# Kernel optimization log

Hardware: AMD Instinct MI355X
Metric: run time of the kernel (lower is better)

## Reference

```python
import jax, jax.numpy as jnp
import numpy as np

D_MODEL = 5120
N_HEADS = 8
D_HEAD = D_MODEL // N_HEADS          # 640
D_ROPE = 16
SPLIT_DIM = D_HEAD - D_ROPE          # 624
D_KV = 128
BATCH, SEQ = 2, 2048
ROPE_SCALE = 40.0


def _rope_cos_sin(seq_len):
    # inv_freq length = D_ROPE//4 (quirk of the original code)
    inv_freq = 1.0 / (10000.0 ** (jnp.arange(0, D_ROPE // 2, 2, dtype=jnp.float32) / (D_ROPE // 2)))
    t = jnp.arange(seq_len, dtype=jnp.float32) / ROPE_SCALE
    freqs = t[:, None] * inv_freq[None, :]            # [S, D_ROPE//4]
    emb = jnp.concatenate([freqs, freqs], axis=-1)    # [S, D_ROPE//2]
    cos = jnp.cos(emb)[None, :, None, :]              # [1,S,1,D_ROPE//2]
    sin = jnp.sin(emb)[None, :, None, :]
    return cos, sin


def _rotate_half(x):
    x1, x2 = jnp.split(x, 2, axis=-1)
    return jnp.concatenate([-x2, x1], axis=-1)


def _apply_rotary(x, cos, sin):
    r = cos.shape[-1]
    x_rot, x_base = x[..., :r], x[..., r:]
    x_rot = x_rot * cos + _rotate_half(x_rot) * sin
    return jnp.concatenate([x_rot, x_base], axis=-1)


def setup_inputs():
    key = jax.random.key(0)
    ks = jax.random.split(key, 18)
    s = 0.02
    inp = {
        'h': jax.random.normal(ks[0], (BATCH, SEQ, D_MODEL), dtype=jnp.float32),
        'W_dkv': jax.random.normal(ks[1], (D_MODEL, D_KV), dtype=jnp.float32) * s,
        'b_dkv': jnp.zeros((D_KV,), jnp.float32),
        'W_dq': jax.random.normal(ks[2], (D_MODEL, D_KV), dtype=jnp.float32) * s,
        'b_dq': jnp.zeros((D_KV,), jnp.float32),
        'W_uk': jax.random.normal(ks[3], (D_KV, N_HEADS * SPLIT_DIM), dtype=jnp.float32) * s,
        'b_uk': jnp.zeros((N_HEADS * SPLIT_DIM,), jnp.float32),
        'W_uv': jax.random.normal(ks[4], (D_KV, N_HEADS * D_HEAD), dtype=jnp.float32) * s,
        'b_uv': jnp.zeros((N_HEADS * D_HEAD,), jnp.float32),
        'W_uq': jax.random.normal(ks[5], (D_KV, N_HEADS * SPLIT_DIM), dtype=jnp.float32) * s,
        'b_uq': jnp.zeros((N_HEADS * SPLIT_DIM,), jnp.float32),
        'W_qr': jax.random.normal(ks[6], (D_KV, N_HEADS * D_ROPE), dtype=jnp.float32) * s,
        'b_qr': jnp.zeros((N_HEADS * D_ROPE,), jnp.float32),
        'W_kr': jax.random.normal(ks[7], (D_MODEL, N_HEADS * D_ROPE), dtype=jnp.float32) * s,
        'b_kr': jnp.zeros((N_HEADS * D_ROPE,), jnp.float32),
        'W_o': jax.random.normal(ks[8], (N_HEADS * D_HEAD, D_MODEL), dtype=jnp.float32) * s,
        'b_o': jnp.zeros((D_MODEL,), jnp.float32),
    }
    return inp


def reference(h, W_dkv, b_dkv, W_dq, b_dq, W_uk, b_uk, W_uv, b_uv,
              W_uq, b_uq, W_qr, b_qr, W_kr, b_kr, W_o, b_o):
    B, S, _ = h.shape
    c_kv = h @ W_dkv + b_dkv                                   # [B,S,D_KV]
    k = (c_kv @ W_uk + b_uk).reshape(B, S, N_HEADS, SPLIT_DIM)
    v = (c_kv @ W_uv + b_uv).reshape(B, S, N_HEADS, D_HEAD)
    c_q = h @ W_dq + b_dq
    q_base = (c_q @ W_uq + b_uq).reshape(B, S, N_HEADS, SPLIT_DIM)
    q_rot = (c_q @ W_qr + b_qr).reshape(B, S, N_HEADS, D_ROPE)
    cos, sin = _rope_cos_sin(S)
    q_rot = _apply_rotary(q_rot, cos, sin)
    k_rot = _apply_rotary((h @ W_kr + b_kr).reshape(B, S, N_HEADS, D_ROPE), cos, sin)
    q = jnp.concatenate([q_base, q_rot], axis=-1)              # [B,S,H,D_HEAD]
    k = jnp.concatenate([k, k_rot], axis=-1)                   # [B,S,H,D_HEAD]
    scores = jnp.einsum('bqhd,bkhd->bhqk', q, k) / jnp.sqrt(jnp.float32(D_HEAD))
    attn = jax.nn.softmax(scores, axis=-1)
    out = jnp.einsum('bhqk,bkhd->bqhd', attn, v)               # [B,S,H,D_HEAD]
    return out.reshape(B, S, N_HEADS * D_HEAD) @ W_o + b_o
```

## Files before the change

kernel.cpp:

```cpp
#include <hip/hip_runtime.h>


typedef unsigned short ushort_t;
typedef __attribute__((ext_vector_type(8)))  short          short8;
typedef __attribute__((ext_vector_type(8)))  unsigned short us8;
typedef __attribute__((ext_vector_type(4)))  float          f32x4;
typedef __attribute__((ext_vector_type(4)))  unsigned int   u32x4;

#define SCALE_ATT 0.0395284707521047f

static __device__ inline unsigned short f2bf(float f) {
  union { float f; unsigned u; } v; v.f = f;
  unsigned r = (v.u + 0x7fffu + ((v.u >> 16) & 1u)) >> 16;
  return (unsigned short)r;
}
static __device__ inline float bf2f(unsigned short u) {
  union { unsigned u; float f; } v; v.u = ((unsigned)u) << 16;
  return v.f;
}
static __device__ inline unsigned cvt_pk_bf16(float a, float b) {
  unsigned r;
  asm("v_cvt_pk_bf16_f32 %0, %1, %2" : "=v"(r) : "v"(a), "v"(b));
  return r;
}
static __device__ inline f32x4 MFMA(short8 a, short8 b, f32x4 c) {
  return __builtin_amdgcn_mfma_f32_16x16x32_bf16(a, b, c, 0, 0, 0);
}

__global__ __launch_bounds__(256) void k_bvec_init(const float* __restrict__ bo,
                                                   float* __restrict__ bvec) {
  int n = blockIdx.x * 256 + threadIdx.x;
  bvec[n] = bo[n];
}

__global__ __launch_bounds__(128) void k_bqabs(const float* __restrict__ buq,
                                               const float* __restrict__ Wuk,
                                               float* __restrict__ bqabs) {
  int h = blockIdx.x, j = threadIdx.x;
  float acc = 0.f;
  const float* bq = buq + h * 624;
  const float* wk = Wuk + (size_t)j * 4992 + h * 624;
  for (int d = 0; d < 624; ++d) acc += bq[d] * wk[d];
  bqabs[h * 128 + j] = acc;
}

__global__ __launch_bounds__(256) void k_wqk(const float* __restrict__ Wuq,
                                             const float* __restrict__ Wuk,
                                             ushort_t* __restrict__ wqkT) {
  __shared__ float Aq[16 * 132];
  __shared__ float Ak[16 * 132];
  int jt = blockIdx.x, it = blockIdx.y, h = blockIdx.z;
  int i0 = it * 16, j0 = jt * 16;
  int t = threadIdx.x;
  int srow = t >> 4, sc0 = (t & 15) * 8;
  int ti = t & 15, tj = t >> 4;
  float acc = 0.f;
  for (int dc = 0; dc < 624; dc += 128) {
#pragma unroll
    for (int i = 0; i < 8; ++i) {
      int d = dc + sc0 + i;
      Aq[srow * 132 + sc0 + i] = (d < 624) ? Wuq[(size_t)(i0 + srow) * 4992 + h * 624 + d] : 0.f;
      Ak[srow * 132 + sc0 + i] = (d < 624) ? Wuk[(size_t)(j0 + srow) * 4992 + h * 624 + d] : 0.f;
    }
    __syncthreads();
    int cs = (624 - dc) < 128 ? (624 - dc) : 128;
    for (int d = 0; d < cs; d += 4) {
      const f32x4 a4 = *(const f32x4*)&Aq[ti * 132 + d];
      const f32x4 b4 = *(const f32x4*)&Ak[tj * 132 + d];
      acc += a4[0] * b4[0] + a4[1] * b4[1] + a4[2] * b4[2] + a4[3] * b4[3];
    }
    __syncthreads();
  }
  wqkT[(size_t)h * 16384 + (size_t)(j0 + tj) * 128 + (i0 + ti)] = f2bf(acc);
}

__global__ __launch_bounds__(256) void k_gemm1_sk(
    const float* __restrict__ H, const float* __restrict__ Wdkv,
    const float* __restrict__ Wdq, const float* __restrict__ Wkr,
    float* __restrict__ part) {
  __shared__ __align__(16) ushort_t As[64 * 72];
  __shared__ __align__(16) ushort_t Bs[192 * 72];
  const int tid = threadIdx.x;
  const int m0 = blockIdx.x * 64;
  const int n0 = blockIdx.y * 192;
  const int kc0 = blockIdx.z * 1280;
  const int lane = tid & 63, wid = tid >> 6;
  const int quad = lane >> 4, l15 = lane & 15;
  f32x4 acc[4][3];
#pragma unroll
  for (int a = 0; a < 4; ++a)
#pragma unroll
    for (int b = 0; b < 3; ++b) acc[a][b] = (f32x4){0.f, 0.f, 0.f, 0.f};
  const int ar = tid >> 2, ak0 = (tid & 3) * 16;
  const int bkp = tid >> 3;
  const int bng = tid & 7;
  const float* harow = H + (size_t)(m0 + ar) * 5120 + ak0;
  for (int kb = kc0; kb < kc0 + 1280; kb += 64) {
    const float* ap = harow + kb;
    f32x4 af0 = *(const f32x4*)ap, af1 = *(const f32x4*)(ap + 4);
    f32x4 af2 = *(const f32x4*)(ap + 8), af3 = *(const f32x4*)(ap + 12);
    u32x4 apk0 = { cvt_pk_bf16(af0[0], af0[1]), cvt_pk_bf16(af0[2], af0[3]),
                   cvt_pk_bf16(af1[0], af1[1]), cvt_pk_bf16(af1[2], af1[3]) };
    u32x4 apk1 = { cvt_pk_bf16(af2[0], af2[1]), cvt_pk_bf16(af2[2], af2[3]),
                   cvt_pk_bf16(af3[0], af3[1]), cvt_pk_bf16(af3[2], af3[3]) };
    *(u32x4*)&As[ar * 72 + ak0] = apk0;
    *(u32x4*)&As[ar * 72 + ak0 + 8] = apk1;
    const int krow = kb + 2 * bkp;
    const int kd = (2 * bkp) ^ (bng << 3);
#pragma unroll
    for (int g = 0; g < 3; ++g) {
      const int lcol = g * 64 + bng * 8;
      const int col = n0 + lcol;
      const float* base = (col < 128 ? Wdkv + col
                         : col < 256 ? Wdq + (col - 128)
                                     : Wkr + (col - 256)) + (size_t)krow * 128;
      f32x4 r0a = *(const f32x4*)base, r0b = *(const f32x4*)(base + 4);
      f32x4 r1a = *(const f32x4*)(base + 128), r1b = *(const f32x4*)(base + 132);
#pragma unroll
      for (int i = 0; i < 4; ++i) {
        *(unsigned*)&Bs[(lcol + i) * 72 + kd]     = cvt_pk_bf16(r0a[i], r1a[i]);
        *(unsigned*)&Bs[(lcol + 4 + i) * 72 + kd] = cvt_pk_bf16(r0b[i], r1b[i]);
      }
    }
    __syncthreads();
#pragma unroll
    for (int ks = 0; ks < 2; ++ks) {
      short8 a[4], b[3];
#pragma unroll
      for (int mt = 0; mt < 4; ++mt)
        a[mt] = *(const short8*)&As[(mt * 16 + l15) * 72 + ks * 32 + quad * 8];
#pragma unroll
      for (int nt = 0; nt < 3; ++nt) {
        const int row = wid * 48 + nt * 16 + l15;
        const int kofs = (ks * 32 + quad * 8) ^ (((row >> 3) & 7) << 3);
        b[nt] = *(const short8*)&Bs[row * 72 + kofs];
      }
#pragma unroll
      for (int mt = 0; mt < 4; ++mt)
#pragma unroll
        for (int nt = 0; nt < 3; ++nt) acc[mt][nt] = MFMA(a[mt], b[nt], acc[mt][nt]);
    }
    __syncthreads();
  }
  const size_t pb = (size_t)blockIdx.z * 4096 * 384;
#pragma unroll
  for (int mt = 0; mt < 4; ++mt)
#pragma unroll
    for (int nt = 0; nt < 3; ++nt) {
      const int col = n0 + wid * 48 + nt * 16 + l15;
#pragma unroll
      for (int r = 0; r < 4; ++r) {
        const int row = m0 + mt * 16 + quad * 4 + r;
        part[pb + (size_t)row * 384 + col] = acc[mt][nt][r];
      }
    }
}

__global__ __launch_bounds__(384) void k_reduce(
    const float* __restrict__ part, const float* __restrict__ bdkv,
    const float* __restrict__ bdq, const float* __restrict__ bkr,
    ushort_t* __restrict__ ckv, ushort_t* __restrict__ cq,
    ushort_t* __restrict__ krot) {
  const int row = blockIdx.x;
  const int c = threadIdx.x;
  float v = 0.f;
#pragma unroll
  for (int ks = 0; ks < 4; ++ks)
    v += part[((size_t)ks * 4096 + row) * 384 + c];
  if (c < 128) {
    v += bdkv[c];
    ckv[(size_t)row * 128 + c] = f2bf(v);
  } else if (c < 256) {
    v += bdq[c - 128];
    cq[(size_t)row * 128 + (c - 128)] = f2bf(v);
  } else {
    v += bkr[c - 256];
    float partner = __shfl_xor(v, 4);
    const int j = (c - 256) & 15;
    const int head = (c - 256) >> 4;
    const int s = row & 2047, bb = row >> 11;
    const int j4 = j & 3;
    const float fr = (j4 == 0) ? 1.f : (j4 == 1) ? 0.1f : (j4 == 2) ? 0.01f : 0.001f;
    float sth, cth;
    __sincosf(s * 0.025f * fr, &sth, &cth);
    const float y = (j < 4) ? (v * cth - partner * sth)
                  : (j < 8) ? (v * cth + partner * sth) : v;
    krot[((size_t)((bb << 3) + head) * 2048 + s) * 16 + j] = f2bf(y);
  }
}

__global__ __launch_bounds__(256) void k_ckvt(const ushort_t* __restrict__ ckv,
                                              ushort_t* __restrict__ ckvT) {
  __shared__ __align__(16) ushort_t T[128 * 72];
  const int tid = threadIdx.x;
  const int s0 = blockIdx.x * 64;
  const int bb = s0 >> 11, sl = s0 & 2047;
  const int sr = tid >> 2, sseg = tid & 3;
  {
    const ushort_t* kp = ckv + ((size_t)s0 + sr) * 128 + sseg * 32;
    us8 v[4];
#pragma unroll
    for (int w = 0; w < 4; ++w) v[w] = *(const us8*)(kp + w * 8);
#pragma unroll
    for (int w = 0; w < 4; ++w)
#pragma unroll
      for (int i = 0; i < 8; ++i)
        T[(sseg * 32 + w * 8 + i) * 72 + sr] = v[w][i];
  }
  __syncthreads();
  const int vrow = tid >> 1, vk0 = (tid & 1) * 32;
#pragma unroll
  for (int w = 0; w < 4; ++w) {
    us8 t = *(const us8*)&T[vrow * 72 + vk0 + w * 8];
    *(us8*)(ckvT + ((size_t)bb * 128 + vrow) * 2048 + sl + vk0 + w * 8) = t;
  }
}

__global__ __launch_bounds__(256) void k_qrot(const ushort_t* __restrict__ cq,
                                              const float* __restrict__ Wqr,
                                              const float* __restrict__ bqr,
                                              ushort_t* __restrict__ qrot) {
  int gidx = blockIdx.x * 256 + threadIdx.x;
  int s = gidx & 2047, bh = gidx >> 11;
  int hh = bh & 7, bb = bh >> 3;
  const ushort_t* crow = cq + ((size_t)bb * 2048 + s) * 128;
  float acc[16];
#pragma unroll
  for (int j = 0; j < 16; ++j) acc[j] = bqr[hh * 16 + j];
  for (int k0 = 0; k0 < 128; k0 += 8) {
    us8 cv8 = *(const us8*)(crow + k0);
#pragma unroll
    for (int i = 0; i < 8; ++i) {
      float cv = bf2f(cv8[i]);
      const float* wr = Wqr + (size_t)(k0 + i) * 128 + hh * 16;
#pragma unroll
      for (int j = 0; j < 16; ++j) acc[j] += cv * wr[j];
    }
  }
  float y[16];
#pragma unroll
  for (int j4 = 0; j4 < 4; ++j4) {
    float fr = (j4 == 0) ? 1.f : (j4 == 1) ? 0.1f : (j4 == 2) ? 0.01f : 0.001f;
    float sth, cth;
    __sincosf(s * 0.025f * fr, &sth, &cth);
    y[j4] = acc[j4] * cth - acc[j4 + 4] * sth;
    y[j4 + 4] = acc[j4 + 4] * cth + acc[j4] * sth;
  }
#pragma unroll
  for (int j = 8; j < 16; ++j) y[j] = acc[j];
  us8 o0, o1;
#pragma unroll
  for (int j = 0; j < 8; ++j) {
    o0[j] = f2bf(y[j] * SCALE_ATT);
    o1[j] = f2bf(y[8 + j] * SCALE_ATT);
  }
  *(us8*)(qrot + (size_t)gidx * 16) = o0;
  *(us8*)(qrot + (size_t)gidx * 16 + 8) = o1;
}

__global__ __launch_bounds__(256) void k_qabs(const ushort_t* __restrict__ cq,
                                              const ushort_t* __restrict__ wqkT,
                                              const float* __restrict__ bqabs,
                                              ushort_t* __restrict__ qabs) {
  __shared__ __align__(16) ushort_t As[128 * 72];
  __shared__ __align__(16) ushort_t Bs[128 * 72];
  const int tid = threadIdx.x;
  const int m0 = blockIdx.x * 128, hh = blockIdx.y;
  const int lane = tid & 63, wid = tid >> 6;
  const int quad = lane >> 4, l15 = lane & 15;
  const int wm = wid & 1, wn = wid >> 1;
  f32x4 acc[4][4];
#pragma unroll
  for (int a = 0; a < 4; ++a)
#pragma unroll
    for (int b = 0; b < 4; ++b) acc[a][b] = (f32x4){0.f, 0.f, 0.f, 0.f};
  const int ar = tid >> 1, as0 = (tid & 1) * 32;
  for (int kb = 0; kb < 128; kb += 64) {
    const ushort_t* ap = cq + (size_t)(m0 + ar) * 128 + kb + as0;
    const ushort_t* bp = wqkT + (size_t)hh * 16384 + (size_t)ar * 128 + kb + as0;
#pragma unroll
    for (int w = 0; w < 4; ++w) {
      *(us8*)&As[ar * 72 + as0 + w * 8] = *(const us8*)(ap + w * 8);
      *(us8*)&Bs[ar * 72 + as0 + w * 8] = *(const us8*)(bp + w * 8);
    }
    __syncthreads();
#pragma unroll
    for (int ks = 0; ks < 2; ++ks) {
      short8 a[4], b[4];
#pragma unroll
      for (int mt = 0; mt < 4; ++mt)
        a[mt] = *(const short8*)&As[(wm * 64 + mt * 16 + l15) * 72 + ks * 32 + quad * 8];
#pragma unroll
      for (int nt = 0; nt < 4; ++nt)
        b[nt] = *(const short8*)&Bs[(wn * 64 + nt * 16 + l15) * 72 + ks * 32 + quad * 8];
#pragma unroll
      for (int mt = 0; mt < 4; ++mt)
#pragma unroll
        for (int nt = 0; nt < 4; ++nt) acc[mt][nt] = MFMA(a[mt], b[nt], acc[mt][nt]);
    }
    __syncthreads();
  }
#pragma unroll
  for (int mt = 0; mt < 4; ++mt)
#pragma unroll
    for (int nt = 0; nt < 4; ++nt) {
      int col = wn * 64 + nt * 16 + l15;
      float bias = bqabs[hh * 128 + col];
#pragma unroll
      for (int r = 0; r < 4; ++r) {
        int m = m0 + wm * 64 + mt * 16 + quad * 4 + r;
        int bb = m >> 11, s = m & 2047;
        qabs[((size_t)((bb << 3) + hh) * 2048 + s) * 128 + col] =
            f2bf((acc[mt][nt][r] + bias) * SCALE_ATT);
      }
    }
}

__global__ __launch_bounds__(256) void k_comb(const float* __restrict__ Wo,
                                              const float* __restrict__ Wuv,
                                              const float* __restrict__ buv,
                                              ushort_t* __restrict__ wcombT,
                                              float* __restrict__ bvec) {
  __shared__ __align__(16) ushort_t As[128 * 72];
  __shared__ __align__(16) ushort_t Bs[128 * 72];
  const int tid = threadIdx.x;
  const int n0 = blockIdx.x * 128, hh = blockIdx.y;
  const int lane = tid & 63, wid = tid >> 6;
  const int quad = lane >> 4, l15 = lane & 15;
  const int wm = wid & 1, wn = wid >> 1;
  f32x4 acc[4][4];
#pragma unroll
  for (int a = 0; a < 4; ++a)
#pragma unroll
    for (int b = 0; b < 4; ++b) acc[a][b] = (f32x4){0.f, 0.f, 0.f, 0.f};
  const int akp = tid >> 3;
  const int ang = tid & 7;
  const int kd0 = (2 * akp) ^ (((2 * ang) & 7) << 3);
  const int kd1 = (2 * akp) ^ (((2 * ang + 1) & 7) << 3);
  const int bc = tid >> 1, bd0 = (tid & 1) * 32;
  const int bvc = tid >> 1, bvh = tid & 1;
  const int bswz = ((bvc >> 3) & 7) << 3;
  const float* buvh = buv + hh * 640;
  float bacc = 0.f;
  for (int kb = 0; kb < 640; kb += 64) {
    {
      const float* ap0 = Wo + (size_t)(hh * 640 + kb + 2 * akp) * 5120 + n0 + ang * 16;
      const float* ap1 = ap0 + 5120;
      f32x4 r0[4], r1[4];
#pragma unroll
      for (int w = 0; w < 4; ++w) {
        r0[w] = *(const f32x4*)(ap0 + w * 4);
        r1[w] = *(const f32x4*)(ap1 + w * 4);
      }
#pragma unroll
      for (int w = 0; w < 2; ++w)
#pragma unroll
        for (int i = 0; i < 4; ++i)
          *(unsigned*)&As[(ang * 16 + w * 4 + i) * 72 + kd0] =
              cvt_pk_bf16(r0[w][i], r1[w][i]);
#pragma unroll
      for (int w = 2; w < 4; ++w)
#pragma unroll
        for (int i = 0; i < 4; ++i)
          *(unsigned*)&As[(ang * 16 + w * 4 + i) * 72 + kd1] =
              cvt_pk_bf16(r0[w][i], r1[w][i]);
    }
    const float* bp = Wuv + (size_t)bc * 5120 + hh * 640 + kb + bd0;
    f32x4 b0 = *(const f32x4*)bp, b1 = *(const f32x4*)(bp + 4);
    f32x4 b2 = *(const f32x4*)(bp + 8), b3 = *(const f32x4*)(bp + 12);
    f32x4 b4 = *(const f32x4*)(bp + 16), b5 = *(const f32x4*)(bp + 20);
    f32x4 b6 = *(const f32x4*)(bp + 24), b7 = *(const f32x4*)(bp + 28);
    u32x4 q0 = { cvt_pk_bf16(b0[0], b0[1]), cvt_pk_bf16(b0[2], b0[3]),
                 cvt_pk_bf16(b1[0], b1[1]), cvt_pk_bf16(b1[2], b1[3]) };
    u32x4 q1 = { cvt_pk_bf16(b2[0], b2[1]), cvt_pk_bf16(b2[2], b2[3]),
                 cvt_pk_bf16(b3[0], b3[1]), cvt_pk_bf16(b3[2], b3[3]) };
    u32x4 q2 = { cvt_pk_bf16(b4[0], b4[1]), cvt_pk_bf16(b4[2], b4[3]),
                 cvt_pk_bf16(b5[0], b5[1]), cvt_pk_bf16(b5[2], b5[3]) };
    u32x4 q3 = { cvt_pk_bf16(b6[0], b6[1]), cvt_pk_bf16(b6[2], b6[3]),
                 cvt_pk_bf16(b7[0], b7[1]), cvt_pk_bf16(b7[2], b7[3]) };
    *(u32x4*)&Bs[bc * 72 + bd0]      = q0;
    *(u32x4*)&Bs[bc * 72 + bd0 + 8]  = q1;
    *(u32x4*)&Bs[bc * 72 + bd0 + 16] = q2;
    *(u32x4*)&Bs[bc * 72 + bd0 + 24] = q3;
    __syncthreads();
#pragma unroll
    for (int d8 = 0; d8 < 4; ++d8) {
      const int k0 = bvh * 32 + d8 * 8;
      const us8 a8 = *(const us8*)&As[bvc * 72 + (k0 ^ bswz)];
      const f32x4 b4a = *(const f32x4*)&buvh[kb + k0];
      const f32x4 b4b = *(const f32x4*)&buvh[kb + k0 + 4];
      bacc += b4a[0] * bf2f(a8[0]) + b4a[1] * bf2f(a8[1]) +
              b4a[2] * bf2f(a8[2]) + b4a[3] * bf2f(a8[3]) +
              b4b[0] * bf2f(a8[4]) + b4b[1] * bf2f(a8[5]) +
              b4b[2] * bf2f(a8[6]) + b4b[3] * bf2f(a8[7]);
    }
#pragma unroll
    for (int ks = 0; ks < 2; ++ks) {
      short8 a[4], b[4];
#pragma unroll
      for (int mt = 0; mt < 4; ++mt) {
        const int row = wm * 64 + mt * 16 + l15;
        const int kofs = (ks * 32 + quad * 8) ^ (((row >> 3) & 7) << 3);
        a[mt] = *(const short8*)&As[row * 72 + kofs];
      }
#pragma unroll
      for (int nt = 0; nt < 4; ++nt)
        b[nt] = *(const short8*)&Bs[(wn * 64 + nt * 16 + l15) * 72 + ks * 32 + quad * 8];
#pragma unroll
      for (int mt = 0; mt < 4; ++mt)
#pragma unroll
        for (int nt = 0; nt < 4; ++nt) acc[mt][nt] = MFMA(a[mt], b[nt], acc[mt][nt]);
    }
    __syncthreads();
  }
#pragma unroll
  for (int mt = 0; mt < 4; ++mt)
#pragma unroll
    for (int nt = 0; nt < 4; ++nt) {
      int col = wn * 64 + nt * 16 + l15;
#pragma unroll
      for (int r = 0; r < 4; ++r) {
        int n = n0 + wm * 64 + mt * 16 + quad * 4 + r;
        wcombT[(size_t)n * 1024 + hh * 128 + col] = f2bf(acc[mt][nt][r]);
      }
    }
  atomicAdd(&bvec[n0 + bvc], bacc);
}

__global__ __launch_bounds__(256) void k_attn(const ushort_t* __restrict__ qabs,
                                              const ushort_t* __restrict__ qrot,
                                              const ushort_t* __restrict__ ckv,
                                              const ushort_t* __restrict__ krot,
                                              const ushort_t* __restrict__ ckvT,
                                              ushort_t* __restrict__ ctx) {
  __shared__ __align__(16) ushort_t Qs[64 * 168];
  __shared__ __align__(16) ushort_t Ks[64 * 168];
  __shared__ __align__(16) ushort_t Vt[128 * 72];
  __shared__ __align__(16) ushort_t Ps[64 * 72];
  const int tid = threadIdx.x;
  const int bh = blockIdx.y, bb = bh >> 3, hh = bh & 7;
  const int q0 = blockIdx.x * 64;
  const int lane = tid & 63, wid = tid >> 6;
  const int quad = lane >> 4, l15 = lane & 15;
  const int sr = tid >> 2, sseg = tid & 3;
  const int vrow = tid >> 1, vk0 = (tid & 1) * 32;
  (void)hh;
  {
    const ushort_t* qa = qabs + ((size_t)bh * 2048 + q0 + sr) * 128 + sseg * 32;
#pragma unroll
    for (int w = 0; w < 4; ++w)
      *(us8*)&Qs[sr * 168 + sseg * 32 + w * 8] = *(const us8*)(qa + w * 8);
    if (sseg == 0) {
      const ushort_t* qr = qrot + ((size_t)bh * 2048 + q0 + sr) * 16;
      *(us8*)&Qs[sr * 168 + 128] = *(const us8*)qr;
      *(us8*)&Qs[sr * 168 + 136] = *(const us8*)(qr + 8);
    }
    if (sseg == 1) {
      us8 z = (us8)0;
      *(us8*)&Qs[sr * 168 + 144] = z;
      *(us8*)&Qs[sr * 168 + 152] = z;
      *(us8*)&Ks[sr * 168 + 144] = z;
      *(us8*)&Ks[sr * 168 + 152] = z;
    }
  }
  us8 kreg[4], vreg[4], krr0, krr1;
  auto loadKV = [&](int key0) {
    const ushort_t* kp = ckv + ((size_t)bb * 2048 + key0 + sr) * 128 + sseg * 32;
#pragma unroll
    for (int w = 0; w < 4; ++w) kreg[w] = *(const us8*)(kp + w * 8);
    const ushort_t* vp = ckvT + ((size_t)bb * 128 + vrow) * 2048 + key0 + vk0;
#pragma unroll
    for (int w = 0; w < 4; ++w) vreg[w] = *(const us8*)(vp + w * 8);
    if (sseg == 0) {
      const ushort_t* kr = krot + ((size_t)bh * 2048 + key0 + sr) * 16;
      krr0 = *(const us8*)kr;
      krr1 = *(const us8*)(kr + 8);
    }
  };
  loadKV(0);
  f32x4 oacc[8];
#pragma unroll
  for (int i = 0; i < 8; ++i) oacc[i] = (f32x4){0.f, 0.f, 0.f, 0.f};
  float mrow[4] = {-1e30f, -1e30f, -1e30f, -1e30f};
  float m_sm = -1e30f;
  float lrow_l = 0.f;

  for (int kt = 0; kt < 32; ++kt) {
#pragma unroll
    for (int w = 0; w < 4; ++w)
      *(us8*)&Ks[sr * 168 + sseg * 32 + w * 8] = kreg[w];
    if (sseg == 0) {
      *(us8*)&Ks[sr * 168 + 128] = krr0;
      *(us8*)&Ks[sr * 168 + 136] = krr1;
    }
#pragma unroll
    for (int w = 0; w < 4; ++w)
      *(us8*)&Vt[vrow * 72 + vk0 + w * 8] = vreg[w];
    __syncthreads();
    f32x4 sacc[4];
#pragma unroll
    for (int nt = 0; nt < 4; ++nt) sacc[nt] = (f32x4){0.f, 0.f, 0.f, 0.f};
#pragma unroll
    for (int ks = 0; ks < 5; ++ks) {
      short8 aq = *(const short8*)&Qs[(wid * 16 + l15) * 168 + ks * 32 + quad * 8];
#pragma unroll
      for (int nt = 0; nt < 4; ++nt) {
        short8 bk = *(const short8*)&Ks[(nt * 16 + l15) * 168 + ks * 32 + quad * 8];
        sacc[nt] = MFMA(bk, aq, sacc[nt]);
      }
    }
    if (kt < 31) loadKV((kt + 1) * 64);
    float mx = sacc[0][0];
#pragma unroll
    for (int nt = 0; nt < 4; ++nt)
#pragma unroll
      for (int r = 0; r < 4; ++r) mx = fmaxf(mx, sacc[nt][r]);
    mx = fmaxf(mx, __shfl_xor(mx, 16));
    mx = fmaxf(mx, __shfl_xor(mx, 32));
    const bool grew = mx > m_sm;
    if (__any(grew)) {
      if (grew) { lrow_l *= __expf(m_sm - mx); m_sm = mx; }
#pragma unroll
      for (int r = 0; r < 4; ++r) {
        float mnew = __shfl(m_sm, quad * 4 + r);
        if (mnew > mrow[r]) {
          float alpha = __expf(mrow[r] - mnew);
          mrow[r] = mnew;
#pragma unroll
          for (int t8 = 0; t8 < 8; ++t8) oacc[t8][r] *= alpha;
        }
      }
    }
    float rs = 0.f;
    const int prow = (wid * 16 + l15) * 72 + quad * 4;
#pragma unroll
    for (int nt = 0; nt < 4; ++nt) {
      float p0 = __expf(sacc[nt][0] - m_sm);
      float p1 = __expf(sacc[nt][1] - m_sm);
      float p2 = __expf(sacc[nt][2] - m_sm);
      float p3 = __expf(sacc[nt][3] - m_sm);
      rs += (p0 + p1) + (p2 + p3);
      *(unsigned*)&Ps[prow + nt * 16]     = cvt_pk_bf16(p0, p1);
      *(unsigned*)&Ps[prow + nt * 16 + 2] = cvt_pk_bf16(p2, p3);
    }
    lrow_l += rs;
#pragma unroll
    for (int kk = 0; kk < 2; ++kk) {
      short8 pa = *(const short8*)&Ps[(wid * 16 + l15) * 72 + kk * 32 + quad * 8];
#pragma unroll
      for (int nt = 0; nt < 8; ++nt) {
        short8 vb = *(const short8*)&Vt[(nt * 16 + l15) * 72 + kk * 32 + quad * 8];
        oacc[nt] = MFMA(pa, vb, oacc[nt]);
      }
    }
    __syncthreads();
  }
  lrow_l += __shfl_xor(lrow_l, 16);
  lrow_l += __shfl_xor(lrow_l, 32);
#pragma unroll
  for (int r = 0; r < 4; ++r) {
    float rl = 1.f / __shfl(lrow_l, quad * 4 + r);
    int row = q0 + wid * 16 + quad * 4 + r;
    size_t base = ((size_t)bb * 2048 + row) * 1024 + hh * 128;
#pragma unroll
    for (int nt = 0; nt < 8; ++nt)
      ctx[base + nt * 16 + l15] = f2bf(oacc[nt][r] * rl);
  }
}

__global__ __launch_bounds__(256) void k_final(const ushort_t* __restrict__ ctx,
                                               const ushort_t* __restrict__ wcombT,
                                               const float* __restrict__ bvec,
                                               float* __restrict__ out) {
  __shared__ __align__(16) ushort_t As[128 * 72];
  __shared__ __align__(16) ushort_t Bs[128 * 72];
  const int tid = threadIdx.x;
  const int m0 = blockIdx.x * 128, n0 = blockIdx.y * 128;
  const int lane = tid & 63, wid = tid >> 6;
  const int quad = lane >> 4, l15 = lane & 15;
  const int wm = wid & 1, wn = wid >> 1;
  f32x4 acc[4][4];
#pragma unroll
  for (int a = 0; a < 4; ++a)
#pragma unroll
    for (int b = 0; b < 4; ++b) acc[a][b] = (f32x4){0.f, 0.f, 0.f, 0.f};
  const int ar = tid >> 1, as0 = (tid & 1) * 32;
  const ushort_t* ap = ctx + (size_t)(m0 + ar) * 1024 + as0;
  const ushort_t* bp = wcombT + (size_t)(n0 + ar) * 1024 + as0;
  us8 ra[4], rb[4];
#pragma unroll
  for (int w = 0; w < 4; ++w) {
    ra[w] = *(const us8*)(ap + w * 8);
    rb[w] = *(const us8*)(bp + w * 8);
  }
  for (int kb = 0; kb < 1024; kb += 64) {
#pragma unroll
    for (int w = 0; w < 4; ++w) {
      *(us8*)&As[ar * 72 + as0 + w * 8] = ra[w];
      *(us8*)&Bs[ar * 72 + as0 + w * 8] = rb[w];
    }
    __syncthreads();
    if (kb < 960) {
      const ushort_t* ap2 = ap + kb + 64;
      const ushort_t* bp2 = bp + kb + 64;
#pragma unroll
      for (int w = 0; w < 4; ++w) {
        ra[w] = *(const us8*)(ap2 + w * 8);
        rb[w] = *(const us8*)(bp2 + w * 8);
      }
    }
#pragma unroll
    for (int ks = 0; ks < 2; ++ks) {
      short8 a[4], b[4];
#pragma unroll
      for (int mt = 0; mt < 4; ++mt)
        a[mt] = *(const short8*)&As[(wm * 64 + mt * 16 + l15) * 72 + ks * 32 + quad * 8];
#pragma unroll
      for (int nt = 0; nt < 4; ++nt)
        b[nt] = *(const short8*)&Bs[(wn * 64 + nt * 16 + l15) * 72 + ks * 32 + quad * 8];
#pragma unroll
      for (int mt = 0; mt < 4; ++mt)
#pragma unroll
        for (int nt = 0; nt < 4; ++nt) acc[mt][nt] = MFMA(a[mt], b[nt], acc[mt][nt]);
    }
    __syncthreads();
  }
#pragma unroll
  for (int mt = 0; mt < 4; ++mt)
#pragma unroll
    for (int nt = 0; nt < 4; ++nt) {
      int col = wn * 64 + nt * 16 + l15;
      float bias = bvec[n0 + col];
#pragma unroll
      for (int r = 0; r < 4; ++r) {
        int row = m0 + wm * 64 + mt * 16 + quad * 4 + r;
        out[(size_t)row * 5120 + n0 + col] = acc[mt][nt][r] + bias;
      }
    }
}

extern "C" void kernel_launch(void* const* d_in, const int* in_sizes, int n_in,
                              void* d_out, int out_size, void* d_ws, size_t ws_size,
                              hipStream_t stream) {
  const float* H    = (const float*)d_in[0];
  const float* Wdkv = (const float*)d_in[1];
  const float* bdkv = (const float*)d_in[2];
  const float* Wdq  = (const float*)d_in[3];
  const float* bdq  = (const float*)d_in[4];
  const float* Wuk  = (const float*)d_in[5];
  const float* Wuv  = (const float*)d_in[7];
  const float* buv  = (const float*)d_in[8];
  const float* Wuq  = (const float*)d_in[9];
  const float* buq  = (const float*)d_in[10];
  const float* Wqr  = (const float*)d_in[11];
  const float* bqr  = (const float*)d_in[12];
  const float* Wkr  = (const float*)d_in[13];
  const float* bkr  = (const float*)d_in[14];
  const float* Wo   = (const float*)d_in[15];
  const float* bo   = (const float*)d_in[16];
  float* out = (float*)d_out;

  char* ws = (char*)d_ws;
  size_t off = 0;
  auto alloc = [&](size_t bytes) -> void* {
    void* p = ws + off;
    off += (bytes + 255) & ~(size_t)255;
    return p;
  };
  ushort_t* ckv    = (ushort_t*)alloc((size_t)4096 * 128 * 2);
  ushort_t* cq     = (ushort_t*)alloc((size_t)4096 * 128 * 2);
  ushort_t* ckvT   = (ushort_t*)alloc((size_t)2 * 128 * 2048 * 2);
  ushort_t* krot   = (ushort_t*)alloc((size_t)16 * 2048 * 16 * 2);
  ushort_t* qrot   = (ushort_t*)alloc((size_t)16 * 2048 * 16 * 2);
  ushort_t* wqkT   = (ushort_t*)alloc((size_t)8 * 128 * 128 * 2);
  float*    bqabs  = (float*)alloc((size_t)8 * 128 * 4);
  float*    bvec   = (float*)alloc((size_t)5120 * 4);
  size_t mark = off;
  float*    part   = (float*)alloc((size_t)4 * 4096 * 384 * 4);
  size_t endB = off;
  off = mark;
  ushort_t* qabs   = (ushort_t*)alloc((size_t)16 * 2048 * 128 * 2);
  ushort_t* wcombT = (ushort_t*)alloc((size_t)5120 * 1024 * 2);
  ushort_t* ctx    = (ushort_t*)alloc((size_t)4096 * 1024 * 2);
  if (off < endB) off = endB;
  (void)ws_size; (void)in_sizes; (void)n_in; (void)out_size;

  hipLaunchKernelGGL(k_bvec_init, dim3(20), dim3(256), 0, stream, bo, bvec);
  hipLaunchKernelGGL(k_bqabs, dim3(8), dim3(128), 0, stream, buq, Wuk, bqabs);
  hipLaunchKernelGGL(k_wqk, dim3(8, 8, 8), dim3(256), 0, stream, Wuq, Wuk, wqkT);
  hipLaunchKernelGGL(k_gemm1_sk, dim3(64, 2, 4), dim3(256), 0, stream,
                     H, Wdkv, Wdq, Wkr, part);
  hipLaunchKernelGGL(k_reduce, dim3(4096), dim3(384), 0, stream,
                     part, bdkv, bdq, bkr, ckv, cq, krot);
  hipLaunchKernelGGL(k_ckvt, dim3(64), dim3(256), 0, stream, ckv, ckvT);
  hipLaunchKernelGGL(k_comb, dim3(40, 8), dim3(256), 0, stream, Wo, Wuv, buv, wcombT, bvec);
  hipLaunchKernelGGL(k_qrot, dim3(128), dim3(256), 0, stream, cq, Wqr, bqr, qrot);
  hipLaunchKernelGGL(k_qabs, dim3(32, 8), dim3(256), 0, stream, cq, wqkT, bqabs, qabs);
  hipLaunchKernelGGL(k_attn, dim3(32, 16), dim3(256), 0, stream,
                     qabs, qrot, ckv, krot, ckvT, ctx);
  hipLaunchKernelGGL(k_final, dim3(32, 40), dim3(256), 0, stream, ctx, wcombT, bvec, out);
}
```

Baseline: 652.6 us.

## Fuse bias-absorb into Wqk precompute and compute it with bf16 MFMA

Replaces the scalar fp32 shared-memory dot-product kernel that builds the per-head absorbed Wuq·Wuk^T matrix with an MFMA bf16 GEMM, one 128x128 block per head. The separate bqabs kernel is folded into the same pass by reusing the loaded Wuk values, which saves a launch and a second read of Wuk. The grid shrinks from 512 blocks to 8, so parallelism drops. The weight product is now rounded through bf16 inputs instead of fp32 accumulation on fp32 data.

```diff
diff --git a/kernel.cpp b/kernel.cpp
--- a/kernel.cpp
+++ b/kernel.cpp
@@ -33,45 +33,105 @@
   bvec[n] = bo[n];
 }
 
-__global__ __launch_bounds__(128) void k_bqabs(const float* __restrict__ buq,
-                                               const float* __restrict__ Wuk,
-                                               float* __restrict__ bqabs) {
-  int h = blockIdx.x, j = threadIdx.x;
-  float acc = 0.f;
-  const float* bq = buq + h * 624;
-  const float* wk = Wuk + (size_t)j * 4992 + h * 624;
-  for (int d = 0; d < 624; ++d) acc += bq[d] * wk[d];
-  bqabs[h * 128 + j] = acc;
-}
-
 __global__ __launch_bounds__(256) void k_wqk(const float* __restrict__ Wuq,
                                              const float* __restrict__ Wuk,
-                                             ushort_t* __restrict__ wqkT) {
-  __shared__ float Aq[16 * 132];
-  __shared__ float Ak[16 * 132];
-  int jt = blockIdx.x, it = blockIdx.y, h = blockIdx.z;
-  int i0 = it * 16, j0 = jt * 16;
-  int t = threadIdx.x;
-  int srow = t >> 4, sc0 = (t & 15) * 8;
-  int ti = t & 15, tj = t >> 4;
-  float acc = 0.f;
-  for (int dc = 0; dc < 624; dc += 128) {
-#pragma unroll
-    for (int i = 0; i < 8; ++i) {
-      int d = dc + sc0 + i;
-      Aq[srow * 132 + sc0 + i] = (d < 624) ? Wuq[(size_t)(i0 + srow) * 4992 + h * 624 + d] : 0.f;
-      Ak[srow * 132 + sc0 + i] = (d < 624) ? Wuk[(size_t)(j0 + srow) * 4992 + h * 624 + d] : 0.f;
-    }
-    __syncthreads();
-    int cs = (624 - dc) < 128 ? (624 - dc) : 128;
-    for (int d = 0; d < cs; d += 4) {
-      const f32x4 a4 = *(const f32x4*)&Aq[ti * 132 + d];
-      const f32x4 b4 = *(const f32x4*)&Ak[tj * 132 + d];
-      acc += a4[0] * b4[0] + a4[1] * b4[1] + a4[2] * b4[2] + a4[3] * b4[3];
-    }
-    __syncthreads();
-  }
-  wqkT[(size_t)h * 16384 + (size_t)(j0 + tj) * 128 + (i0 + ti)] = f2bf(acc);
+                                             const float* __restrict__ buq,
+                                             ushort_t* __restrict__ wqkT,
+                                             float* __restrict__ bqabs) {
+  __shared__ __align__(16) ushort_t As[128 * 72];
+  __shared__ __align__(16) ushort_t Bs[128 * 72];
+  const int tid = threadIdx.x;
+  const int hh = blockIdx.x;
+  const int lane = tid & 63, wid = tid >> 6;
+  const int quad = lane >> 4, l15 = lane & 15;
+  const int wm = wid & 1, wn = wid >> 1;
+  f32x4 acc[4][4];
+#pragma unroll
+  for (int a = 0; a < 4; ++a)
+#pragma unroll
+    for (int b = 0; b < 4; ++b) acc[a][b] = (f32x4){0.f, 0.f, 0.f, 0.f};
+  const int r = tid >> 1, c0 = (tid & 1) * 32;
+  float bacc = 0.f;
+  for (int kb = 0; kb < 640; kb += 64) {
+    const int dbase = kb + c0;
+    const float* ak = Wuk + (size_t)r * 4992 + hh * 624 + dbase;
+    const float* aq = Wuq + (size_t)r * 4992 + hh * 624 + dbase;
+    const float* bu = buq + hh * 624 + dbase;
+    float vk[32], vq[32];
+    if (dbase + 32 <= 624) {
+#pragma unroll
+      for (int w = 0; w < 8; ++w) {
+        const f32x4 t1 = *(const f32x4*)(ak + w * 4);
+        const f32x4 t2 = *(const f32x4*)(aq + w * 4);
+        const f32x4 t3 = *(const f32x4*)(bu + w * 4);
+#pragma unroll
+        for (int e = 0; e < 4; ++e) { vk[w * 4 + e] = t1[e]; vq[w * 4 + e] = t2[e]; }
+        bacc += t3[0] * t1[0] + t3[1] * t1[1] + t3[2] * t1[2] + t3[3] * t1[3];
+      }
+    } else {
+#pragma unroll
+      for (int i2 = 0; i2 < 32; ++i2) {
+        const bool ok = (dbase + i2) < 624;
+        const float wkv = ok ? ak[i2] : 0.f;
+        vk[i2] = wkv;
+        vq[i2] = ok ? aq[i2] : 0.f;
+        bacc += (ok ? bu[i2] : 0.f) * wkv;
+      }
+    }
+    u32x4 pk0 = { cvt_pk_bf16(vk[0], vk[1]),  cvt_pk_bf16(vk[2], vk[3]),
+                  cvt_pk_bf16(vk[4], vk[5]),  cvt_pk_bf16(vk[6], vk[7]) };
+    u32x4 pk1 = { cvt_pk_bf16(vk[8], vk[9]),  cvt_pk_bf16(vk[10], vk[11]),
+                  cvt_pk_bf16(vk[12], vk[13]), cvt_pk_bf16(vk[14], vk[15]) };
+    u32x4 pk2 = { cvt_pk_bf16(vk[16], vk[17]), cvt_pk_bf16(vk[18], vk[19]),
+                  cvt_pk_bf16(vk[20], vk[21]), cvt_pk_bf16(vk[22], vk[23]) };
+    u32x4 pk3 = { cvt_pk_bf16(vk[24], vk[25]), cvt_pk_bf16(vk[26], vk[27]),
+                  cvt_pk_bf16(vk[28], vk[29]), cvt_pk_bf16(vk[30], vk[31]) };
+    *(u32x4*)&As[r * 72 + c0]      = pk0;
+    *(u32x4*)&As[r * 72 + c0 + 8]  = pk1;
+    *(u32x4*)&As[r * 72 + c0 + 16] = pk2;
+    *(u32x4*)&As[r * 72 + c0 + 24] = pk3;
+    u32x4 pq0 = { cvt_pk_bf16(vq[0], vq[1]),  cvt_pk_bf16(vq[2], vq[3]),
+                  cvt_pk_bf16(vq[4], vq[5]),  cvt_pk_bf16(vq[6], vq[7]) };
+    u32x4 pq1 = { cvt_pk_bf16(vq[8], vq[9]),  cvt_pk_bf16(vq[10], vq[11]),
+                  cvt_pk_bf16(vq[12], vq[13]), cvt_pk_bf16(vq[14], vq[15]) };
+    u32x4 pq2 = { cvt_pk_bf16(vq[16], vq[17]), cvt_pk_bf16(vq[18], vq[19]),
+                  cvt_pk_bf16(vq[20], vq[21]), cvt_pk_bf16(vq[22], vq[23]) };
+    u32x4 pq3 = { cvt_pk_bf16(vq[24], vq[25]), cvt_pk_bf16(vq[26], vq[27]),
+                  cvt_pk_bf16(vq[28], vq[29]), cvt_pk_bf16(vq[30], vq[31]) };
+    *(u32x4*)&Bs[r * 72 + c0]      = pq0;
+    *(u32x4*)&Bs[r * 72 + c0 + 8]  = pq1;
+    *(u32x4*)&Bs[r * 72 + c0 + 16] = pq2;
+    *(u32x4*)&Bs[r * 72 + c0 + 24] = pq3;
+    __syncthreads();
+#pragma unroll
+    for (int ks = 0; ks < 2; ++ks) {
+      short8 a[4], b[4];
+#pragma unroll
+      for (int mt = 0; mt < 4; ++mt)
+        a[mt] = *(const short8*)&As[(wm * 64 + mt * 16 + l15) * 72 + ks * 32 + quad * 8];
+#pragma unroll
+      for (int nt = 0; nt < 4; ++nt)
+        b[nt] = *(const short8*)&Bs[(wn * 64 + nt * 16 + l15) * 72 + ks * 32 + quad * 8];
+#pragma unroll
+      for (int mt = 0; mt < 4; ++mt)
+#pragma unroll
+        for (int nt = 0; nt < 4; ++nt) acc[mt][nt] = MFMA(a[mt], b[nt], acc[mt][nt]);
+    }
+    __syncthreads();
+  }
+#pragma unroll
+  for (int mt = 0; mt < 4; ++mt)
+#pragma unroll
+    for (int nt = 0; nt < 4; ++nt) {
+      const int i = wn * 64 + nt * 16 + l15;
+#pragma unroll
+      for (int rr = 0; rr < 4; ++rr) {
+        const int j = wm * 64 + mt * 16 + quad * 4 + rr;
+        wqkT[(size_t)hh * 16384 + (size_t)j * 128 + i] = f2bf(acc[mt][nt][rr]);
+      }
+    }
+  const float po = __shfl_xor(bacc, 1);
+  if ((tid & 1) == 0) bqabs[hh * 128 + r] = bacc + po;
 }
 
 __global__ __launch_bounds__(256) void k_gemm1_sk(
@@ -686,8 +746,7 @@
   (void)ws_size; (void)in_sizes; (void)n_in; (void)out_size;
 
   hipLaunchKernelGGL(k_bvec_init, dim3(20), dim3(256), 0, stream, bo, bvec);
-  hipLaunchKernelGGL(k_bqabs, dim3(8), dim3(128), 0, stream, buq, Wuk, bqabs);
-  hipLaunchKernelGGL(k_wqk, dim3(8, 8, 8), dim3(256), 0, stream, Wuq, Wuk, wqkT);
+  hipLaunchKernelGGL(k_wqk, dim3(8), dim3(256), 0, stream, Wuq, Wuk, buq, wqkT, bqabs);
   hipLaunchKernelGGL(k_gemm1_sk, dim3(64, 2, 4), dim3(256), 0, stream,
                      H, Wdkv, Wdq, Wkr, part);
   hipLaunchKernelGGL(k_reduce, dim3(4096), dim3(384), 0, stream,
```

Result: faster. 577.6 us (-11.5%).
